# Kernel optimization log

Hardware: AMD Instinct MI355X
Metric: run time of the kernel (lower is better)

## Reference

```python
import jax, jax.numpy as jnp
import numpy as np

N, E, G = 50000, 600000, 256
D, L, V = 128, 5, 128
BN_EPS = 1e-5


def setup_inputs() -> dict:
    key = jax.random.key(0)
    ks = jax.random.split(key, 24)
    x = jax.random.randint(ks[0], (N, 9), 0, V)
    edge_index = jax.random.randint(ks[1], (2, E), 0, N)
    edge_attr = jax.random.randint(ks[2], (E, 3), 0, V)
    batch = jnp.sort(jax.random.randint(ks[3], (N,), 0, G))
    s = 0.02
    inp = dict(
        x=x, edge_index=edge_index, edge_attr=edge_attr, batch=batch,
        atom_emb=jax.random.normal(ks[4], (9, V, D)) * s,
        bond_emb=jax.random.normal(ks[5], (L, 3, V, D)) * s,
        eps=jnp.zeros((L,)),
        W1=jax.random.normal(ks[6], (D, 2 * D)) * s, b1=jnp.zeros((2 * D,)),
        g1=jnp.ones((2 * D,)), be1=jnp.zeros((2 * D,)),
        W2=jax.random.normal(ks[7], (2 * D, D)) * s, b2=jnp.zeros((D,)),
        bn_g=jnp.ones((L, D)), bn_b=jnp.zeros((L, D)),
        fcW1=jax.random.normal(ks[8], (D, 1024)) * s, fcb1=jnp.zeros((1024,)),
        fcW2=jax.random.normal(ks[9], (1024, 1024)) * s, fcb2=jnp.zeros((1024,)),
        fcW3=jax.random.normal(ks[10], (1024, 512)) * s, fcb3=jnp.zeros((512,)),
        fcW4=jax.random.normal(ks[11], (512, 1)) * s, fcb4=jnp.zeros((1,)),
    )
    return inp


def _bn(h, g, b):
    # training-mode batchnorm (biased variance, as torch uses for normalization)
    m = h.mean(0)
    v = jnp.var(h, axis=0)
    return (h - m) * jax.lax.rsqrt(v + BN_EPS) * g + b


def _embed(tables, idx):
    # tables: [F, V, D], idx: [M, F] -> sum over F of table lookups -> [M, D]
    F = tables.shape[0]
    return tables[jnp.arange(F)[None, :], idx].sum(axis=1)


def reference(x, edge_index, edge_attr, batch, atom_emb, bond_emb, eps,
              W1, b1, g1, be1, W2, b2, bn_g, bn_b,
              fcW1, fcb1, fcW2, fcb2, fcW3, fcb3, fcW4, fcb4):
    src, dst = edge_index[0], edge_index[1]

    def mlp(h):
        z = jax.nn.relu(_bn(h @ W1 + b1, g1, be1))
        return z @ W2 + b2

    h = _embed(atom_emb, x)  # AtomEncoder: [N, D]
    h_sum = h  # JK='sum' accumulator
    for l in range(L):
        e = _embed(bond_emb[l], edge_attr)            # BondEncoder: [E, D]
        msg = jax.nn.relu(h[src] + e)                  # gather + elementwise
        agg = jax.ops.segment_sum(msg, dst, num_segments=N)  # scatter-add
        h = mlp((1.0 + eps[l]) * h + agg)
        h = _bn(h, bn_g[l], bn_b[l])
        if l < L - 1:
            h = jax.nn.relu(h)
        # dropout is identity in eval mode
        h_sum = h_sum + h

    # global mean pool over graphs
    sums = jax.ops.segment_sum(h_sum, batch, num_segments=G)
    cnts = jax.ops.segment_sum(jnp.ones((N,), h_sum.dtype), batch, num_segments=G)
    rep = sums / jnp.maximum(cnts, 1.0)[:, None]

    z = jax.nn.relu(rep @ fcW1 + fcb1)
    z = jax.nn.relu(z @ fcW2 + fcb2)
    z = jax.nn.relu(z @ fcW3 + fcb3)
    out = (z @ fcW4 + fcb4).squeeze(-1)  # [G]
    return out
```

## Files before the change

### kernel.cpp

```cpp
#include <hip/hip_runtime.h>

typedef unsigned short u16;
typedef unsigned int u32;
typedef __bf16 bf16x8 __attribute__((ext_vector_type(8)));
typedef float f32x4 __attribute__((ext_vector_type(4)));

#define NN 50000
#define EE 600000
#define GG 256
#define LL 5
#define NB 196

__device__ __forceinline__ float b2f(u16 u) {
  unsigned int v = ((unsigned int)u) << 16;
  return __builtin_bit_cast(float, v);
}
__device__ __forceinline__ u16 f2b(float f) {
  unsigned int u = __builtin_bit_cast(unsigned int, f);
  u += 0x7FFFu + ((u >> 16) & 1u);
  return (u16)(u >> 16);
}

__global__ void k_detect(const u32* __restrict__ w, int* __restrict__ flag) {
  __shared__ int sh[256];
  u32 v = w[threadIdx.x];
  u32 lo = v & 0xFFFFu;
  u32 e = (lo >> 7) & 0xFFu;
  sh[threadIdx.x] = (e >= 0x60u && e <= 0x7Fu) ? 1 : 0;
  __syncthreads();
  for (int s = 128; s > 0; s >>= 1) {
    if (threadIdx.x < (unsigned)s) sh[threadIdx.x] += sh[threadIdx.x + s];
    __syncthreads();
  }
  if (threadIdx.x == 0) flag[0] = (sh[0] < 128) ? 1 : 0;
}

struct CvtArgs {
  const void* src[19];
  u16* dst[19];
  int cum[20];
};

__global__ void k_cvt_all(CvtArgs a, const int* __restrict__ flag) {
  int t = blockIdx.x * 256 + threadIdx.x;
  if (t >= a.cum[19]) return;
  int i = 0;
  while (t >= a.cum[i + 1]) ++i;
  int j = t - a.cum[i];
  if (flag[0]) a.dst[i][j] = f2b(((const float*)a.src[i])[j]);
  else a.dst[i][j] = ((const u16*)a.src[i])[j];
}

__global__ void k_tr(const u16* __restrict__ src, u16* __restrict__ dst, int K, int N) {
  int idx = blockIdx.x * 256 + threadIdx.x;
  if (idx >= K * N) return;
  int n = idx / K, k = idx - n * K;
  dst[idx] = src[k * N + n];
}

__global__ void k_deg(const int* __restrict__ ei, int* __restrict__ deg) {
  int e = blockIdx.x * 256 + threadIdx.x;
  if (e < EE) atomicAdd(&deg[ei[EE + e]], 1);
}

__global__ void k_scan1(const int* __restrict__ deg, int* __restrict__ rowp,
                        int* __restrict__ bsum) {
  __shared__ int sh[256];
  int i = blockIdx.x * 256 + threadIdx.x;
  int v = (i < NN) ? deg[i] : 0;
  sh[threadIdx.x] = v;
  __syncthreads();
  for (int s = 1; s < 256; s <<= 1) {
    int t = (threadIdx.x >= (unsigned)s) ? sh[threadIdx.x - s] : 0;
    __syncthreads();
    sh[threadIdx.x] += t;
    __syncthreads();
  }
  if (i < NN) rowp[i] = sh[threadIdx.x] - v;
  if (threadIdx.x == 255) bsum[blockIdx.x] = sh[255];
}

__global__ void k_scan2(int* __restrict__ bsum, int* __restrict__ boff) {
  __shared__ int sh[256];
  int v = (threadIdx.x < NB) ? bsum[threadIdx.x] : 0;
  sh[threadIdx.x] = v;
  __syncthreads();
  for (int s = 1; s < 256; s <<= 1) {
    int t = (threadIdx.x >= (unsigned)s) ? sh[threadIdx.x - s] : 0;
    __syncthreads();
    sh[threadIdx.x] += t;
    __syncthreads();
  }
  if (threadIdx.x < NB) boff[threadIdx.x] = sh[threadIdx.x] - v;
}

__global__ void k_scan3(int* __restrict__ rowp, const int* __restrict__ boff,
                        int* __restrict__ cursor) {
  int i = blockIdx.x * 256 + threadIdx.x;
  if (i < NN) {
    int r = rowp[i] + boff[blockIdx.x];
    rowp[i] = r;
    cursor[i] = r;
  }
  if (i == 0) rowp[NN] = EE;
}

__global__ void k_fill(const int* __restrict__ ei, const int* __restrict__ eattr,
                       int* __restrict__ cursor, uint2* __restrict__ epack) {
  int e = blockIdx.x * 256 + threadIdx.x;
  if (e < EE) {
    int d = ei[EE + e];
    int pos = atomicAdd(&cursor[d], 1);
    u32 src = (u32)ei[e];
    u32 a0 = (u32)eattr[e * 3], a1 = (u32)eattr[e * 3 + 1], a2 = (u32)eattr[e * 3 + 2];
    epack[pos] = make_uint2(src | (a0 << 16) | (a1 << 23), a2);
  }
}

__global__ void k_gb(const int* __restrict__ batch, int* __restrict__ gstart,
                     int* __restrict__ gend) {
  int n = blockIdx.x * 256 + threadIdx.x;
  if (n < NN) {
    int b = batch[n];
    atomicMin(&gstart[b], n);
    atomicMax(&gend[b], n);
  }
}

__global__ void k_atom(const int* __restrict__ x, const u16* __restrict__ aemb,
                       u16* __restrict__ h) {
  int idx = blockIdx.x * 256 + threadIdx.x;
  if (idx >= NN * 64) return;
  int n = idx >> 6, f2 = (idx & 63) << 1;
  float a0 = 0.f, a1 = 0.f;
#pragma unroll
  for (int j = 0; j < 9; ++j) {
    int xv = x[n * 9 + j];
    u32 v = *(const u32*)(aemb + (j * 128 + xv) * 128 + f2);
    a0 += b2f((u16)v);
    a1 += b2f((u16)(v >> 16));
  }
  u32 o = (u32)f2b(a0) | ((u32)f2b(a1) << 16);
  *(u32*)(h + n * 128 + f2) = o;
}

__global__ __launch_bounds__(256)
void k_pull(const u16* __restrict__ h, const int* __restrict__ rowp,
            const uint2* __restrict__ epack, const u16* __restrict__ bond,
            const u16* __restrict__ epsv, int layer, u16* __restrict__ amat) {
  const int lane = threadIdx.x & 63;
  const int node = blockIdx.x * 4 + (threadIdx.x >> 6);
  const int p0 = rowp[node], p1 = rowp[node + 1];
  const int lo = lane << 1;
  const u16* bondB = bond + 16384;
  const u16* bondC = bond + 32768;
  float acc0 = 0.f, acc1 = 0.f;
  int p = p0;
  for (; p + 4 <= p1; p += 4) {
    uint2 e0 = epack[p], e1 = epack[p + 1], e2 = epack[p + 2], e3 = epack[p + 3];
    u32 h0 = *(const u32*)(h + (size_t)(e0.x & 0xFFFFu) * 128 + lo);
    u32 h1 = *(const u32*)(h + (size_t)(e1.x & 0xFFFFu) * 128 + lo);
    u32 h2 = *(const u32*)(h + (size_t)(e2.x & 0xFFFFu) * 128 + lo);
    u32 h3 = *(const u32*)(h + (size_t)(e3.x & 0xFFFFu) * 128 + lo);
    u32 a0 = *(const u32*)(bond + ((e0.x >> 16) & 0x7Fu) * 128 + lo);
    u32 a1 = *(const u32*)(bond + ((e1.x >> 16) & 0x7Fu) * 128 + lo);
    u32 a2 = *(const u32*)(bond + ((e2.x >> 16) & 0x7Fu) * 128 + lo);
    u32 a3 = *(const u32*)(bond + ((e3.x >> 16) & 0x7Fu) * 128 + lo);
    u32 b0 = *(const u32*)(bondB + ((e0.x >> 23) & 0x7Fu) * 128 + lo);
    u32 b1 = *(const u32*)(bondB + ((e1.x >> 23) & 0x7Fu) * 128 + lo);
    u32 b2 = *(const u32*)(bondB + ((e2.x >> 23) & 0x7Fu) * 128 + lo);
    u32 b3 = *(const u32*)(bondB + ((e3.x >> 23) & 0x7Fu) * 128 + lo);
    u32 c0 = *(const u32*)(bondC + e0.y * 128 + lo);
    u32 c1 = *(const u32*)(bondC + e1.y * 128 + lo);
    u32 c2 = *(const u32*)(bondC + e2.y * 128 + lo);
    u32 c3 = *(const u32*)(bondC + e3.y * 128 + lo);
    acc0 += fmaxf(b2f((u16)h0) + b2f((u16)a0) + b2f((u16)b0) + b2f((u16)c0), 0.f);
    acc1 += fmaxf(b2f((u16)(h0 >> 16)) + b2f((u16)(a0 >> 16)) + b2f((u16)(b0 >> 16)) + b2f((u16)(c0 >> 16)), 0.f);
    acc0 += fmaxf(b2f((u16)h1) + b2f((u16)a1) + b2f((u16)b1) + b2f((u16)c1), 0.f);
    acc1 += fmaxf(b2f((u16)(h1 >> 16)) + b2f((u16)(a1 >> 16)) + b2f((u16)(b1 >> 16)) + b2f((u16)(c1 >> 16)), 0.f);
    acc0 += fmaxf(b2f((u16)h2) + b2f((u16)a2) + b2f((u16)b2) + b2f((u16)c2), 0.f);
    acc1 += fmaxf(b2f((u16)(h2 >> 16)) + b2f((u16)(a2 >> 16)) + b2f((u16)(b2 >> 16)) + b2f((u16)(c2 >> 16)), 0.f);
    acc0 += fmaxf(b2f((u16)h3) + b2f((u16)a3) + b2f((u16)b3) + b2f((u16)c3), 0.f);
    acc1 += fmaxf(b2f((u16)(h3 >> 16)) + b2f((u16)(a3 >> 16)) + b2f((u16)(b3 >> 16)) + b2f((u16)(c3 >> 16)), 0.f);
  }
  for (; p < p1; ++p) {
    uint2 e0 = epack[p];
    u32 h0 = *(const u32*)(h + (size_t)(e0.x & 0xFFFFu) * 128 + lo);
    u32 a0 = *(const u32*)(bond + ((e0.x >> 16) & 0x7Fu) * 128 + lo);
    u32 b0 = *(const u32*)(bondB + ((e0.x >> 23) & 0x7Fu) * 128 + lo);
    u32 c0 = *(const u32*)(bondC + e0.y * 128 + lo);
    acc0 += fmaxf(b2f((u16)h0) + b2f((u16)a0) + b2f((u16)b0) + b2f((u16)c0), 0.f);
    acc1 += fmaxf(b2f((u16)(h0 >> 16)) + b2f((u16)(a0 >> 16)) + b2f((u16)(b0 >> 16)) + b2f((u16)(c0 >> 16)), 0.f);
  }
  float epsf = 1.0f + b2f(epsv[layer]);
  u32 own = *(const u32*)(h + (size_t)node * 128 + lo);
  u32 o = (u32)f2b(epsf * b2f((u16)own) + acc0) |
          ((u32)f2b(epsf * b2f((u16)(own >> 16)) + acc1) << 16);
  *(u32*)(amat + (size_t)node * 128 + lo) = o;
}

__global__ __launch_bounds__(256)
void k_gemm1(const u16* __restrict__ amat, const u16* __restrict__ w1t,
             const u16* __restrict__ b1, u16* __restrict__ z0,
             float* __restrict__ bnsum, float* __restrict__ bnsq) {
  __shared__ u16 As[128 * 72];
  __shared__ u16 Bs[128 * 72];
  __shared__ float colAcc[256];
  const int tid = threadIdx.x;
  const int r0 = blockIdx.x * 128;
  const int nc = blockIdx.y * 128;
  const int w = tid >> 6, lane = tid & 63, l15 = lane & 15, q = lane >> 4;
  const int wr = (w & 1) * 64, wc = (w >> 1) * 64;
  f32x4 acc[4][4];
#pragma unroll
  for (int i = 0; i < 4; ++i)
#pragma unroll
    for (int j = 0; j < 4; ++j) acc[i][j] = {0.f, 0.f, 0.f, 0.f};

#pragma unroll
  for (int ks = 0; ks < 2; ++ks) {
    const int k0 = ks * 64;
    for (int idx = tid; idx < 1024; idx += 256) {
      const int row = idx >> 3, c8 = (idx & 7) << 3;
      int gr = r0 + row; if (gr >= NN) gr = NN - 1;
      uint4 va = *(const uint4*)(amat + (size_t)gr * 128 + k0 + c8);
      *(uint4*)(As + row * 72 + c8) = va;
      uint4 vb = *(const uint4*)(w1t + (size_t)(nc + row) * 128 + k0 + c8);
      *(uint4*)(Bs + row * 72 + c8) = vb;
    }
    __syncthreads();
#pragma unroll
    for (int kk = 0; kk < 64; kk += 32) {
      const int kf = kk + q * 8;
      bf16x8 a[4], b[4];
#pragma unroll
      for (int i = 0; i < 4; ++i) a[i] = *(const bf16x8*)(As + (wr + i * 16 + l15) * 72 + kf);
#pragma unroll
      for (int j = 0; j < 4; ++j) b[j] = *(const bf16x8*)(Bs + (wc + j * 16 + l15) * 72 + kf);
#pragma unroll
      for (int i = 0; i < 4; ++i)
#pragma unroll
        for (int j = 0; j < 4; ++j)
          acc[i][j] = __builtin_amdgcn_mfma_f32_16x16x32_bf16(a[i], b[j], acc[i][j], 0, 0, 0);
    }
    __syncthreads();
  }
  colAcc[tid] = 0.f;
  __syncthreads();
#pragma unroll
  for (int j = 0; j < 4; ++j) {
    const int c = wc + j * 16 + l15;
    const float bias = b2f(b1[nc + c]);
    float ls = 0.f, lsq = 0.f;
#pragma unroll
    for (int i = 0; i < 4; ++i) {
      const int gr = r0 + wr + i * 16 + q * 4;
#pragma unroll
      for (int rg = 0; rg < 4; ++rg) {
        if (gr + rg < NN) {
          const float v = acc[i][j][rg] + bias;
          z0[(gr + rg) * 256 + nc + c] = f2b(v);
          ls += v;
          lsq += v * v;
        }
      }
    }
    atomicAdd(&colAcc[c], ls);
    atomicAdd(&colAcc[128 + c], lsq);
  }
  __syncthreads();
  if (tid < 128) {
    atomicAdd(&bnsum[nc + tid], colAcc[tid]);
    atomicAdd(&bnsq[nc + tid], colAcc[128 + tid]);
  }
}

__global__ void k_bnfin(float* __restrict__ bnsum, float* __restrict__ bnsq,
                        const u16* __restrict__ g, const u16* __restrict__ b,
                        float* __restrict__ c1, float* __restrict__ c0) {
  int t = threadIdx.x;
  float s = bnsum[t], q = bnsq[t];
  bnsum[t] = 0.f;
  bnsq[t] = 0.f;
  float m = s * (1.0f / NN);
  float var = q * (1.0f / NN) - m * m;
  float rs = rsqrtf(var + 1e-5f);
  float cc1 = rs * b2f(g[t]);
  c1[t] = cc1;
  c0[t] = b2f(b[t]) - m * cc1;
}

__global__ __launch_bounds__(256)
void k_gemm2(const u16* __restrict__ z0, const float* __restrict__ c1,
             const float* __restrict__ c0, const u16* __restrict__ w2t,
             const u16* __restrict__ b2, u16* __restrict__ hpre,
             float* __restrict__ bnsum, float* __restrict__ bnsq) {
  __shared__ u16 As[128 * 72];
  __shared__ u16 Bs[128 * 72];
  __shared__ float colAcc[256];
  const int tid = threadIdx.x;
  const int r0 = blockIdx.x * 128;
  const int w = tid >> 6, lane = tid & 63, l15 = lane & 15, q = lane >> 4;
  const int wr = (w & 1) * 64, wc = (w >> 1) * 64;
  f32x4 acc[4][4];
#pragma unroll
  for (int i = 0; i < 4; ++i)
#pragma unroll
    for (int j = 0; j < 4; ++j) acc[i][j] = {0.f, 0.f, 0.f, 0.f};

#pragma unroll
  for (int ks = 0; ks < 4; ++ks) {
    const int k0 = ks * 64;
    for (int idx = tid; idx < 1024; idx += 256) {
      const int row = idx >> 3, c8 = (idx & 7) << 3;
      int gr = r0 + row; if (gr >= NN) gr = NN - 1;
      ushort4 z01 = *(const ushort4*)(z0 + (size_t)gr * 256 + k0 + c8);
      ushort4 z23 = *(const ushort4*)(z0 + (size_t)gr * 256 + k0 + c8 + 4);
      ushort4 o01, o23;
      {
        const int k = k0 + c8;
        o01.x = f2b(fmaxf(b2f(z01.x) * c1[k + 0] + c0[k + 0], 0.f));
        o01.y = f2b(fmaxf(b2f(z01.y) * c1[k + 1] + c0[k + 1], 0.f));
        o01.z = f2b(fmaxf(b2f(z01.z) * c1[k + 2] + c0[k + 2], 0.f));
        o01.w = f2b(fmaxf(b2f(z01.w) * c1[k + 3] + c0[k + 3], 0.f));
        o23.x = f2b(fmaxf(b2f(z23.x) * c1[k + 4] + c0[k + 4], 0.f));
        o23.y = f2b(fmaxf(b2f(z23.y) * c1[k + 5] + c0[k + 5], 0.f));
        o23.z = f2b(fmaxf(b2f(z23.z) * c1[k + 6] + c0[k + 6], 0.f));
        o23.w = f2b(fmaxf(b2f(z23.w) * c1[k + 7] + c0[k + 7], 0.f));
      }
      *(ushort4*)(As + row * 72 + c8) = o01;
      *(ushort4*)(As + row * 72 + c8 + 4) = o23;
      uint4 vb = *(const uint4*)(w2t + (size_t)row * 256 + k0 + c8);
      *(uint4*)(Bs + row * 72 + c8) = vb;
    }
    __syncthreads();
#pragma unroll
    for (int kk = 0; kk < 64; kk += 32) {
      const int kf = kk + q * 8;
      bf16x8 a[4], b[4];
#pragma unroll
      for (int i = 0; i < 4; ++i) a[i] = *(const bf16x8*)(As + (wr + i * 16 + l15) * 72 + kf);
#pragma unroll
      for (int j = 0; j < 4; ++j) b[j] = *(const bf16x8*)(Bs + (wc + j * 16 + l15) * 72 + kf);
#pragma unroll
      for (int i = 0; i < 4; ++i)
#pragma unroll
        for (int j = 0; j < 4; ++j)
          acc[i][j] = __builtin_amdgcn_mfma_f32_16x16x32_bf16(a[i], b[j], acc[i][j], 0, 0, 0);
    }
    __syncthreads();
  }
  colAcc[tid] = 0.f;
  __syncthreads();
#pragma unroll
  for (int j = 0; j < 4; ++j) {
    const int c = wc + j * 16 + l15;
    const float bias = b2f(b2[c]);
    float ls = 0.f, lsq = 0.f;
#pragma unroll
    for (int i = 0; i < 4; ++i) {
      const int gr = r0 + wr + i * 16 + q * 4;
#pragma unroll
      for (int rg = 0; rg < 4; ++rg) {
        if (gr + rg < NN) {
          const float v = acc[i][j][rg] + bias;
          hpre[(gr + rg) * 128 + c] = f2b(v);
          ls += v;
          lsq += v * v;
        }
      }
    }
    atomicAdd(&colAcc[c], ls);
    atomicAdd(&colAcc[128 + c], lsq);
  }
  __syncthreads();
  if (tid < 128) {
    atomicAdd(&bnsum[tid], colAcc[tid]);
    atomicAdd(&bnsq[tid], colAcc[128 + tid]);
  }
}

__global__ void k_bnapply(const u16* __restrict__ hpre, const float* __restrict__ c1,
                          const float* __restrict__ c0, u16* __restrict__ h, int dorelu) {
  int idx4 = (blockIdx.x * 256 + threadIdx.x) * 4;
  if (idx4 >= NN * 128) return;
  int f = idx4 & 127;
  const ushort4 hv = *(const ushort4*)(hpre + idx4);
  const float4 rv = *(const float4*)(c1 + f);
  const float4 bv = *(const float4*)(c0 + f);
  float v0 = b2f(hv.x) * rv.x + bv.x;
  float v1 = b2f(hv.y) * rv.y + bv.y;
  float v2 = b2f(hv.z) * rv.z + bv.z;
  float v3 = b2f(hv.w) * rv.w + bv.w;
  if (dorelu) {
    v0 = fmaxf(v0, 0.f); v1 = fmaxf(v1, 0.f);
    v2 = fmaxf(v2, 0.f); v3 = fmaxf(v3, 0.f);
  }
  ushort4 ov;
  ov.x = f2b(v0); ov.y = f2b(v1); ov.z = f2b(v2); ov.w = f2b(v3);
  *(ushort4*)(h + idx4) = ov;
}

__global__ void k_poolseg(const u16* __restrict__ h, const int* __restrict__ gstart,
                          const int* __restrict__ gend, float* __restrict__ rep) {
  int g = blockIdx.x >> 2, part = blockIdx.x & 3, f = threadIdx.x;
  int r0 = gstart[g], r1 = gend[g] + 1;
  int len = r1 - r0;
  if (len <= 0) return;
  int chunk = (len + 3) >> 2;
  int s = r0 + part * chunk;
  int e = s + chunk; if (e > r1) e = r1;
  float acc = 0.f;
  for (int r = s; r < e; ++r) acc += b2f(h[r * 128 + f]);
  if (s < e) atomicAdd(&rep[g * 128 + f], acc);
}

__global__ void k_rep(float* __restrict__ rep, const int* __restrict__ gstart,
                      const int* __restrict__ gend, u16* __restrict__ repb) {
  int idx = blockIdx.x * 256 + threadIdx.x;
  int g = idx >> 7;
  int c = gend[g] - gstart[g] + 1;
  if (c < 1) c = 1;
  float v = rep[idx] / (float)c;
  rep[idx] = v;
  repb[idx] = f2b(v);
}

__global__ __launch_bounds__(256)
void k_fcg(const u16* __restrict__ A, const u16* __restrict__ Wt,
           const u16* __restrict__ bias, u16* __restrict__ out, int K, int N) {
  const int tid = threadIdx.x;
  const int r0 = blockIdx.x * 128;
  const int nc = blockIdx.y * 128;
  const int w = tid >> 6, lane = tid & 63, l15 = lane & 15, q = lane >> 4;
  const int wr = (w & 1) * 64, wc = (w >> 1) * 64;
  f32x4 acc[4][4];
#pragma unroll
  for (int i = 0; i < 4; ++i)
#pragma unroll
    for (int j = 0; j < 4; ++j) acc[i][j] = {0.f, 0.f, 0.f, 0.f};
  const int nkb = K >> 5;
  for (int kb = 0; kb < nkb; ++kb) {
    const int kf = kb * 32 + q * 8;
    bf16x8 a[4], b[4];
#pragma unroll
    for (int i = 0; i < 4; ++i)
      a[i] = *(const bf16x8*)(A + (size_t)(r0 + wr + i * 16 + l15) * K + kf);
#pragma unroll
    for (int j = 0; j < 4; ++j)
      b[j] = *(const bf16x8*)(Wt + (size_t)(nc + wc + j * 16 + l15) * K + kf);
#pragma unroll
    for (int i = 0; i < 4; ++i)
#pragma unroll
      for (int j = 0; j < 4; ++j)
        acc[i][j] = __builtin_amdgcn_mfma_f32_16x16x32_bf16(a[i], b[j], acc[i][j], 0, 0, 0);
  }
#pragma unroll
  for (int j = 0; j < 4; ++j) {
    const int c = nc + wc + j * 16 + l15;
    const float bv = b2f(bias[c]);
#pragma unroll
    for (int i = 0; i < 4; ++i) {
      const int gr = r0 + wr + i * 16 + q * 4;
#pragma unroll
      for (int rg = 0; rg < 4; ++rg)
        out[(gr + rg) * N + c] = f2b(fmaxf(acc[i][j][rg] + bv, 0.f));
    }
  }
}

__global__ void k_fc4(const u16* __restrict__ z, const u16* __restrict__ W,
                      const u16* __restrict__ bias, void* __restrict__ out,
                      const int* __restrict__ flag) {
  int g = blockIdx.x, lane = threadIdx.x;
  float acc = 0.f;
  for (int k = lane; k < 512; k += 64) acc += b2f(z[g * 512 + k]) * b2f(W[k]);
  for (int off = 32; off > 0; off >>= 1) acc += __shfl_down(acc, off);
  if (lane == 0) {
    float r = acc + b2f(bias[0]);
    if (flag[0]) ((float*)out)[g] = r;
    else ((u16*)out)[g] = f2b(r);
  }
}

extern "C" void kernel_launch(void* const* d_in, const int* in_sizes, int n_in,
                              void* d_out, int out_size, void* d_ws, size_t ws_size,
                              hipStream_t stream) {
  const int* x     = (const int*)d_in[0];
  const int* ei    = (const int*)d_in[1];
  const int* eattr = (const int*)d_in[2];
  const int* batch = (const int*)d_in[3];

  char* ws = (char*)d_ws;
  size_t off = 0;
  auto alloc = [&](size_t bytes) -> void* {
    void* p = ws + off;
    off += (bytes + 255) & ~(size_t)255;
    return p;
  };
  int* flag = (int*)alloc(256);
  u16* cvt[23];
  CvtArgs ca;
  ca.cum[0] = 0;
  for (int i = 4; i <= 22; ++i) {
    cvt[i] = (u16*)alloc((size_t)in_sizes[i] * 2);
    ca.src[i - 4] = d_in[i];
    ca.dst[i - 4] = cvt[i];
    ca.cum[i - 3] = ca.cum[i - 4] + in_sizes[i];
  }

  u16*   h      = (u16*)  alloc((size_t)NN * 128 * 2);
  u16*   amat   = (u16*)  alloc((size_t)NN * 128 * 2);
  u16*   z0     = (u16*)  alloc((size_t)NN * 256 * 2);
  u16*   w1t    = (u16*)  alloc(32768 * 2);
  u16*   w2t    = (u16*)  alloc(32768 * 2);
  u16*   ft1    = (u16*)  alloc((size_t)1024 * 128 * 2);
  u16*   ft2    = (u16*)  alloc((size_t)1024 * 1024 * 2);
  u16*   ft3    = (u16*)  alloc((size_t)512 * 1024 * 2);
  int*   deg    = (int*)  alloc((size_t)NN * 4);
  int*   cursor = (int*)  alloc((size_t)NN * 4);
  int*   rowp   = (int*)  alloc((size_t)(NN + 1) * 4);
  int*   bsum   = (int*)  alloc((size_t)NB * 4);
  int*   boff   = (int*)  alloc((size_t)NB * 4);
  uint2* epack  = (uint2*)alloc((size_t)EE * 8);
  float* bnbuf  = (float*)alloc(768 * 4);
  float* bnstat = (float*)alloc(1152 * 4);
  float* rep    = (float*)alloc((size_t)GG * 128 * 4);
  u16*   repb   = (u16*)  alloc((size_t)GG * 128 * 2);
  int*   gstart = (int*)  alloc((size_t)GG * 4);
  int*   gend   = (int*)  alloc((size_t)GG * 4);
  u16*   fz1    = (u16*)  alloc((size_t)GG * 1024 * 2);
  u16*   fz2    = (u16*)  alloc((size_t)GG * 1024 * 2);
  u16*   fz3    = (u16*)  alloc((size_t)GG * 512 * 2);
  (void)ws_size; (void)n_in; (void)out_size;

  u16* hpre = amat;

  float* bn1sum = bnbuf;
  float* bn1sq  = bnbuf + 256;
  float* bn2sum = bnbuf + 512;
  float* bn2sq  = bnbuf + 640;
  float* c1a    = bnstat;
  float* c0a    = bnstat + 256;
  float* c1b    = bnstat + 512;
  float* c0b    = bnstat + 640;

  k_detect<<<1, 256, 0, stream>>>((const u32*)d_in[4], flag);
  {
    int total = ca.cum[19];
    k_cvt_all<<<(total + 255) / 256, 256, 0, stream>>>(ca, flag);
  }
  const u16 *aembc = cvt[4], *bembc = cvt[5], *epsc = cvt[6], *w1c = cvt[7],
            *b1c = cvt[8], *g1c = cvt[9], *be1c = cvt[10], *w2c = cvt[11],
            *b2c = cvt[12], *bngc = cvt[13], *bnbc = cvt[14], *fw1 = cvt[15],
            *fb1 = cvt[16], *fw2 = cvt[17], *fb2 = cvt[18], *fw3 = cvt[19],
            *fb3 = cvt[20], *fw4 = cvt[21], *fb4 = cvt[22];

  k_tr<<<128, 256, 0, stream>>>(w1c, w1t, 128, 256);
  k_tr<<<128, 256, 0, stream>>>(w2c, w2t, 256, 128);
  k_tr<<<512, 256, 0, stream>>>(fw1, ft1, 128, 1024);
  k_tr<<<4096, 256, 0, stream>>>(fw2, ft2, 1024, 1024);
  k_tr<<<2048, 256, 0, stream>>>(fw3, ft3, 1024, 512);

  hipMemsetAsync(deg, 0, (size_t)NN * 4, stream);
  hipMemsetAsync(rep, 0, (size_t)GG * 128 * 4, stream);
  hipMemsetAsync(gstart, 0x7F, (size_t)GG * 4, stream);
  hipMemsetAsync(gend, 0xFF, (size_t)GG * 4, stream);
  hipMemsetAsync(bnbuf, 0, 768 * 4, stream);
  k_deg<<<(EE + 255) / 256, 256, 0, stream>>>(ei, deg);
  k_scan1<<<NB, 256, 0, stream>>>(deg, rowp, bsum);
  k_scan2<<<1, 256, 0, stream>>>(bsum, boff);
  k_scan3<<<NB, 256, 0, stream>>>(rowp, boff, cursor);
  k_fill<<<(EE + 255) / 256, 256, 0, stream>>>(ei, eattr, cursor, epack);
  k_gb<<<(NN + 255) / 256, 256, 0, stream>>>(batch, gstart, gend);
  k_atom<<<(NN * 64 + 255) / 256, 256, 0, stream>>>(x, aembc, h);
  k_poolseg<<<GG * 4, 128, 0, stream>>>(h, gstart, gend, rep);

  const int gx = (NN + 127) / 128;
  for (int l = 0; l < LL; ++l) {
    k_pull<<<(NN + 3) / 4, 256, 0, stream>>>(h, rowp, epack,
                                             bembc + (size_t)l * 3 * 128 * 128, epsc, l, amat);
    dim3 grid1(gx, 2);
    k_gemm1<<<grid1, 256, 0, stream>>>(amat, w1t, b1c, z0, bn1sum, bn1sq);
    k_bnfin<<<1, 256, 0, stream>>>(bn1sum, bn1sq, g1c, be1c, c1a, c0a);
    k_gemm2<<<gx, 256, 0, stream>>>(z0, c1a, c0a, w2t, b2c, hpre, bn2sum, bn2sq);
    k_bnfin<<<1, 128, 0, stream>>>(bn2sum, bn2sq, bngc + l * 128, bnbc + l * 128,
                                   c1b, c0b);
    k_bnapply<<<(NN * 128) / 1024, 256, 0, stream>>>(hpre, c1b, c0b, h,
                                                     (l < LL - 1) ? 1 : 0);
    k_poolseg<<<GG * 4, 128, 0, stream>>>(h, gstart, gend, rep);
  }

  k_rep<<<(GG * 128) / 256, 256, 0, stream>>>(rep, gstart, gend, repb);
  {
    dim3 g1(2, 8), g2(2, 8), g3(2, 4);
    k_fcg<<<g1, 256, 0, stream>>>(repb, ft1, fb1, fz1, 128, 1024);
    k_fcg<<<g2, 256, 0, stream>>>(fz1, ft2, fb2, fz2, 1024, 1024);
    k_fcg<<<g3, 256, 0, stream>>>(fz2, ft3, fb3, fz3, 1024, 512);
  }
  k_fc4<<<GG, 64, 0, stream>>>(fz3, fw4, fb4, d_out, flag);
}
```

Measured before the change: 1.028 ms.

## Stage bond tables in LDS and split pull by feature halves

The edge-aggregation kernel now copies a 64-feature slice of the three bond embedding tables into shared memory, splits the feature dimension across two grid columns, and uses a persistent grid with two half-waves processing alternating edges before a shuffle reduction. Separately, the weight transpose uses a tiled LDS kernel, the memsets are fused into one init kernel, graph bounds use neighbour comparison instead of atomics, and the GEMMs get occupancy hints. The intent is to remove global traffic for bond lookups and reduce small-launch overhead. The cost is 48KB of LDS per block, which limits occupancy, plus a repeated table load per block and narrower row gathers.

```diff
diff --git a/kernel.cpp b/kernel.cpp
--- a/kernel.cpp
+++ b/kernel.cpp
@@ -52,10 +52,24 @@
 }
 
 __global__ void k_tr(const u16* __restrict__ src, u16* __restrict__ dst, int K, int N) {
-  int idx = blockIdx.x * 256 + threadIdx.x;
-  if (idx >= K * N) return;
-  int n = idx / K, k = idx - n * K;
-  dst[idx] = src[k * N + n];
+  __shared__ u16 t[32][33];
+  const int kb = blockIdx.x * 32, nb = blockIdx.y * 32;
+  const int tx = threadIdx.x & 31, ty = threadIdx.x >> 5;
+#pragma unroll
+  for (int i = ty; i < 32; i += 8) t[i][tx] = src[(kb + i) * N + nb + tx];
+  __syncthreads();
+#pragma unroll
+  for (int i = ty; i < 32; i += 8) dst[(nb + i) * K + kb + tx] = t[tx][i];
+}
+
+__global__ void k_init(int* __restrict__ deg, float* __restrict__ rep,
+                       float* __restrict__ bnbuf, int* __restrict__ gstart,
+                       int* __restrict__ gend) {
+  int i = blockIdx.x * 256 + threadIdx.x;
+  if (i < NN) deg[i] = 0;
+  if (i < GG * 128) rep[i] = 0.f;
+  if (i < 768) bnbuf[i] = 0.f;
+  if (i < GG) { gstart[i] = 0; gend[i] = -1; }
 }
 
 __global__ void k_deg(const int* __restrict__ ei, int* __restrict__ deg) {
@@ -120,11 +134,10 @@
 __global__ void k_gb(const int* __restrict__ batch, int* __restrict__ gstart,
                      int* __restrict__ gend) {
   int n = blockIdx.x * 256 + threadIdx.x;
-  if (n < NN) {
-    int b = batch[n];
-    atomicMin(&gstart[b], n);
-    atomicMax(&gend[b], n);
-  }
+  if (n >= NN) return;
+  int b = batch[n];
+  if (n == 0 || batch[n - 1] != b) gstart[b] = n;
+  if (n == NN - 1 || batch[n + 1] != b) gend[b] = n;
 }
 
 __global__ void k_atom(const int* __restrict__ x, const u16* __restrict__ aemb,
@@ -148,58 +161,70 @@
 void k_pull(const u16* __restrict__ h, const int* __restrict__ rowp,
             const uint2* __restrict__ epack, const u16* __restrict__ bond,
             const u16* __restrict__ epsv, int layer, u16* __restrict__ amat) {
+  __shared__ u16 sb[3 * 128 * 64];
+  const int f0 = blockIdx.y * 64;
+  for (int i = threadIdx.x; i < 12288; i += 256) {
+    const int row = i >> 5, c2 = (i & 31) << 1;
+    *(u32*)(sb + row * 64 + c2) = *(const u32*)(bond + row * 128 + f0 + c2);
+  }
+  __syncthreads();
+
   const int lane = threadIdx.x & 63;
-  const int node = blockIdx.x * 4 + (threadIdx.x >> 6);
-  const int p0 = rowp[node], p1 = rowp[node + 1];
-  const int lo = lane << 1;
-  const u16* bondB = bond + 16384;
-  const u16* bondC = bond + 32768;
-  float acc0 = 0.f, acc1 = 0.f;
-  int p = p0;
-  for (; p + 4 <= p1; p += 4) {
-    uint2 e0 = epack[p], e1 = epack[p + 1], e2 = epack[p + 2], e3 = epack[p + 3];
-    u32 h0 = *(const u32*)(h + (size_t)(e0.x & 0xFFFFu) * 128 + lo);
-    u32 h1 = *(const u32*)(h + (size_t)(e1.x & 0xFFFFu) * 128 + lo);
-    u32 h2 = *(const u32*)(h + (size_t)(e2.x & 0xFFFFu) * 128 + lo);
-    u32 h3 = *(const u32*)(h + (size_t)(e3.x & 0xFFFFu) * 128 + lo);
-    u32 a0 = *(const u32*)(bond + ((e0.x >> 16) & 0x7Fu) * 128 + lo);
-    u32 a1 = *(const u32*)(bond + ((e1.x >> 16) & 0x7Fu) * 128 + lo);
-    u32 a2 = *(const u32*)(bond + ((e2.x >> 16) & 0x7Fu) * 128 + lo);
-    u32 a3 = *(const u32*)(bond + ((e3.x >> 16) & 0x7Fu) * 128 + lo);
-    u32 b0 = *(const u32*)(bondB + ((e0.x >> 23) & 0x7Fu) * 128 + lo);
-    u32 b1 = *(const u32*)(bondB + ((e1.x >> 23) & 0x7Fu) * 128 + lo);
-    u32 b2 = *(const u32*)(bondB + ((e2.x >> 23) & 0x7Fu) * 128 + lo);
-    u32 b3 = *(const u32*)(bondB + ((e3.x >> 23) & 0x7Fu) * 128 + lo);
-    u32 c0 = *(const u32*)(bondC + e0.y * 128 + lo);
-    u32 c1 = *(const u32*)(bondC + e1.y * 128 + lo);
-    u32 c2 = *(const u32*)(bondC + e2.y * 128 + lo);
-    u32 c3 = *(const u32*)(bondC + e3.y * 128 + lo);
-    acc0 += fmaxf(b2f((u16)h0) + b2f((u16)a0) + b2f((u16)b0) + b2f((u16)c0), 0.f);
-    acc1 += fmaxf(b2f((u16)(h0 >> 16)) + b2f((u16)(a0 >> 16)) + b2f((u16)(b0 >> 16)) + b2f((u16)(c0 >> 16)), 0.f);
-    acc0 += fmaxf(b2f((u16)h1) + b2f((u16)a1) + b2f((u16)b1) + b2f((u16)c1), 0.f);
-    acc1 += fmaxf(b2f((u16)(h1 >> 16)) + b2f((u16)(a1 >> 16)) + b2f((u16)(b1 >> 16)) + b2f((u16)(c1 >> 16)), 0.f);
-    acc0 += fmaxf(b2f((u16)h2) + b2f((u16)a2) + b2f((u16)b2) + b2f((u16)c2), 0.f);
-    acc1 += fmaxf(b2f((u16)(h2 >> 16)) + b2f((u16)(a2 >> 16)) + b2f((u16)(b2 >> 16)) + b2f((u16)(c2 >> 16)), 0.f);
-    acc0 += fmaxf(b2f((u16)h3) + b2f((u16)a3) + b2f((u16)b3) + b2f((u16)c3), 0.f);
-    acc1 += fmaxf(b2f((u16)(h3 >> 16)) + b2f((u16)(a3 >> 16)) + b2f((u16)(b3 >> 16)) + b2f((u16)(c3 >> 16)), 0.f);
-  }
-  for (; p < p1; ++p) {
-    uint2 e0 = epack[p];
-    u32 h0 = *(const u32*)(h + (size_t)(e0.x & 0xFFFFu) * 128 + lo);
-    u32 a0 = *(const u32*)(bond + ((e0.x >> 16) & 0x7Fu) * 128 + lo);
-    u32 b0 = *(const u32*)(bondB + ((e0.x >> 23) & 0x7Fu) * 128 + lo);
-    u32 c0 = *(const u32*)(bondC + e0.y * 128 + lo);
-    acc0 += fmaxf(b2f((u16)h0) + b2f((u16)a0) + b2f((u16)b0) + b2f((u16)c0), 0.f);
-    acc1 += fmaxf(b2f((u16)(h0 >> 16)) + b2f((u16)(a0 >> 16)) + b2f((u16)(b0 >> 16)) + b2f((u16)(c0 >> 16)), 0.f);
-  }
-  float epsf = 1.0f + b2f(epsv[layer]);
-  u32 own = *(const u32*)(h + (size_t)node * 128 + lo);
-  u32 o = (u32)f2b(epsf * b2f((u16)own) + acc0) |
-          ((u32)f2b(epsf * b2f((u16)(own >> 16)) + acc1) << 16);
-  *(u32*)(amat + (size_t)node * 128 + lo) = o;
-}
-
-__global__ __launch_bounds__(256)
+  const int wid = threadIdx.x >> 6;
+  const int half = lane >> 5;
+  const int fl = (lane & 31) << 1;
+  const float epsf = 1.0f + b2f(epsv[layer]);
+
+  for (int node = blockIdx.x * 4 + wid; node < NN; node += gridDim.x * 4) {
+    const int p0 = rowp[node], p1 = rowp[node + 1];
+    float acc0 = 0.f, acc1 = 0.f;
+    int p = p0 + half;
+    while (p < p1) {
+      const bool v1 = (p + 2) < p1, v2 = (p + 4) < p1, v3 = (p + 6) < p1;
+      uint2 e0 = epack[p];
+      uint2 e1 = v1 ? epack[p + 2] : e0;
+      uint2 e2 = v2 ? epack[p + 4] : e0;
+      uint2 e3 = v3 ? epack[p + 6] : e0;
+      u32 h0 = *(const u32*)(h + (size_t)(e0.x & 0xFFFFu) * 128 + f0 + fl);
+      u32 h1 = *(const u32*)(h + (size_t)(e1.x & 0xFFFFu) * 128 + f0 + fl);
+      u32 h2 = *(const u32*)(h + (size_t)(e2.x & 0xFFFFu) * 128 + f0 + fl);
+      u32 h3 = *(const u32*)(h + (size_t)(e3.x & 0xFFFFu) * 128 + f0 + fl);
+      u32 a0 = *(const u32*)(sb + ((e0.x >> 16) & 0x7Fu) * 64 + fl);
+      u32 a1 = *(const u32*)(sb + ((e1.x >> 16) & 0x7Fu) * 64 + fl);
+      u32 a2 = *(const u32*)(sb + ((e2.x >> 16) & 0x7Fu) * 64 + fl);
+      u32 a3 = *(const u32*)(sb + ((e3.x >> 16) & 0x7Fu) * 64 + fl);
+      u32 b0 = *(const u32*)(sb + (8192 + ((e0.x >> 23) & 0x7Fu) * 64) + fl);
+      u32 b1 = *(const u32*)(sb + (8192 + ((e1.x >> 23) & 0x7Fu) * 64) + fl);
+      u32 b2 = *(const u32*)(sb + (8192 + ((e2.x >> 23) & 0x7Fu) * 64) + fl);
+      u32 b3 = *(const u32*)(sb + (8192 + ((e3.x >> 23) & 0x7Fu) * 64) + fl);
+      u32 c0 = *(const u32*)(sb + (16384 + e0.y * 64) + fl);
+      u32 c1 = *(const u32*)(sb + (16384 + e1.y * 64) + fl);
+      u32 c2 = *(const u32*)(sb + (16384 + e2.y * 64) + fl);
+      u32 c3 = *(const u32*)(sb + (16384 + e3.y * 64) + fl);
+      float w0l = fmaxf(b2f((u16)h0) + b2f((u16)a0) + b2f((u16)b0) + b2f((u16)c0), 0.f);
+      float w0h = fmaxf(b2f((u16)(h0 >> 16)) + b2f((u16)(a0 >> 16)) + b2f((u16)(b0 >> 16)) + b2f((u16)(c0 >> 16)), 0.f);
+      float w1l = fmaxf(b2f((u16)h1) + b2f((u16)a1) + b2f((u16)b1) + b2f((u16)c1), 0.f);
+      float w1h = fmaxf(b2f((u16)(h1 >> 16)) + b2f((u16)(a1 >> 16)) + b2f((u16)(b1 >> 16)) + b2f((u16)(c1 >> 16)), 0.f);
+      float w2l = fmaxf(b2f((u16)h2) + b2f((u16)a2) + b2f((u16)b2) + b2f((u16)c2), 0.f);
+      float w2h = fmaxf(b2f((u16)(h2 >> 16)) + b2f((u16)(a2 >> 16)) + b2f((u16)(b2 >> 16)) + b2f((u16)(c2 >> 16)), 0.f);
+      float w3l = fmaxf(b2f((u16)h3) + b2f((u16)a3) + b2f((u16)b3) + b2f((u16)c3), 0.f);
+      float w3h = fmaxf(b2f((u16)(h3 >> 16)) + b2f((u16)(a3 >> 16)) + b2f((u16)(b3 >> 16)) + b2f((u16)(c3 >> 16)), 0.f);
+      acc0 += w0l + (v1 ? w1l : 0.f) + (v2 ? w2l : 0.f) + (v3 ? w3l : 0.f);
+      acc1 += w0h + (v1 ? w1h : 0.f) + (v2 ? w2h : 0.f) + (v3 ? w3h : 0.f);
+      p += 8;
+    }
+    acc0 += __shfl_xor(acc0, 32);
+    acc1 += __shfl_xor(acc1, 32);
+    if (half == 0) {
+      u32 own = *(const u32*)(h + (size_t)node * 128 + f0 + fl);
+      u32 o = (u32)f2b(epsf * b2f((u16)own) + acc0) |
+              ((u32)f2b(epsf * b2f((u16)(own >> 16)) + acc1) << 16);
+      *(u32*)(amat + (size_t)node * 128 + f0 + fl) = o;
+    }
+  }
+}
+
+__global__ __launch_bounds__(256, 2)
 void k_gemm1(const u16* __restrict__ amat, const u16* __restrict__ w1t,
              const u16* __restrict__ b1, u16* __restrict__ z0,
              float* __restrict__ bnsum, float* __restrict__ bnsq) {
@@ -290,7 +315,7 @@
   c0[t] = b2f(b[t]) - m * cc1;
 }
 
-__global__ __launch_bounds__(256)
+__global__ __launch_bounds__(256, 2)
 void k_gemm2(const u16* __restrict__ z0, const float* __restrict__ c1,
              const float* __restrict__ c0, const u16* __restrict__ w2t,
              const u16* __restrict__ b2, u16* __restrict__ hpre,
@@ -556,17 +581,16 @@
             *fb1 = cvt[16], *fw2 = cvt[17], *fb2 = cvt[18], *fw3 = cvt[19],
             *fb3 = cvt[20], *fw4 = cvt[21], *fb4 = cvt[22];
 
-  k_tr<<<128, 256, 0, stream>>>(w1c, w1t, 128, 256);
-  k_tr<<<128, 256, 0, stream>>>(w2c, w2t, 256, 128);
-  k_tr<<<512, 256, 0, stream>>>(fw1, ft1, 128, 1024);
-  k_tr<<<4096, 256, 0, stream>>>(fw2, ft2, 1024, 1024);
-  k_tr<<<2048, 256, 0, stream>>>(fw3, ft3, 1024, 512);
-
-  hipMemsetAsync(deg, 0, (size_t)NN * 4, stream);
-  hipMemsetAsync(rep, 0, (size_t)GG * 128 * 4, stream);
-  hipMemsetAsync(gstart, 0x7F, (size_t)GG * 4, stream);
-  hipMemsetAsync(gend, 0xFF, (size_t)GG * 4, stream);
-  hipMemsetAsync(bnbuf, 0, 768 * 4, stream);
+  {
+    dim3 t1(4, 8), t2(8, 4), t3(4, 32), t4(32, 32), t5(32, 16);
+    k_tr<<<t1, 256, 0, stream>>>(w1c, w1t, 128, 256);
+    k_tr<<<t2, 256, 0, stream>>>(w2c, w2t, 256, 128);
+    k_tr<<<t3, 256, 0, stream>>>(fw1, ft1, 128, 1024);
+    k_tr<<<t4, 256, 0, stream>>>(fw2, ft2, 1024, 1024);
+    k_tr<<<t5, 256, 0, stream>>>(fw3, ft3, 1024, 512);
+  }
+
+  k_init<<<(NN + 255) / 256, 256, 0, stream>>>(deg, rep, bnbuf, gstart, gend);
   k_deg<<<(EE + 255) / 256, 256, 0, stream>>>(ei, deg);
   k_scan1<<<NB, 256, 0, stream>>>(deg, rowp, bsum);
   k_scan2<<<1, 256, 0, stream>>>(bsum, boff);
@@ -578,8 +602,9 @@
 
   const int gx = (NN + 127) / 128;
   for (int l = 0; l < LL; ++l) {
-    k_pull<<<(NN + 3) / 4, 256, 0, stream>>>(h, rowp, epack,
-                                             bembc + (size_t)l * 3 * 128 * 128, epsc, l, amat);
+    dim3 pg(512, 2);
+    k_pull<<<pg, 256, 0, stream>>>(h, rowp, epack,
+                                   bembc + (size_t)l * 3 * 128 * 128, epsc, l, amat);
     dim3 grid1(gx, 2);
     k_gemm1<<<grid1, 256, 0, stream>>>(amat, w1t, b1c, z0, bn1sum, bn1sq);
     k_bnfin<<<1, 256, 0, stream>>>(bn1sum, bn1sq, g1c, be1c, c1a, c0a);
```

New measurement: 1.428 ms. 1.39x slower.
